# Performance work log

Measured on AMD Instinct MI355X. Metric: run time of the kernel, lower is better.

Reference implementation:

```python
import jax, jax.numpy as jnp
import numpy as np

KERNEL_SIZE = 4  # kernel_size=4, dim=1, degree-1 open B-splines (SplineConv defaults)


def spline_conv(x, edge_index, edge_attr, W, root, bias):
    """SplineConv with dim=1, kernel_size=4, degree=1, open splines, aggr='mean'.

    x: [N, F_in]; edge_index: [2, E] (row 0 = source, row 1 = target);
    edge_attr: [E, 1] pseudo-coords in [0,1]; W: [K, F_in, F_out];
    root: [F_in, F_out]; bias: [F_out].
    """
    N = x.shape[0]
    src, dst = edge_index[0], edge_index[1]
    u = edge_attr[:, 0]                          # [E]
    v = u * (KERNEL_SIZE - 1)                    # open spline: scale by K-1
    vf = jnp.floor(v)
    frac = v - vf                                # [E], degree-1 basis fraction
    k0 = jnp.clip(vf.astype(jnp.int32), 0, KERNEL_SIZE - 1)
    k1 = jnp.minimum(k0 + 1, KERNEL_SIZE - 1)
    # Project node features through all K kernel weights once: [N, K, F_out]
    xw = jnp.einsum('nf,kfo->nko', x, W)
    # Per-edge message: basis-weighted mix of the two active kernel projections
    m = (1.0 - frac)[:, None] * xw[src, k0] + frac[:, None] * xw[src, k1]  # [E, F_out]
    # Mean aggregation at target nodes
    agg = jax.ops.segment_sum(m, dst, num_segments=N)               # [N, F_out]
    deg = jax.ops.segment_sum(jnp.ones_like(u), dst, num_segments=N)
    agg = agg / jnp.maximum(deg, 1.0)[:, None]
    return agg + x @ root + bias


def setup_inputs() -> dict:
    key = jax.random.key(0)
    ks = jax.random.split(key, 9)
    N, E, F_IN, HID, C = 50000, 1600000, 48, 32, 10
    x = jax.random.normal(ks[0], (N, F_IN), dtype=jnp.float32)
    edge_index = jax.random.randint(ks[1], (2, E), 0, N, dtype=jnp.int64)
    edge_attr = jax.random.uniform(ks[2], (E, 1), dtype=jnp.float32)
    s = 0.1
    W1 = jax.random.normal(ks[3], (KERNEL_SIZE, F_IN, HID), dtype=jnp.float32) * s
    root1 = jax.random.normal(ks[4], (F_IN, HID), dtype=jnp.float32) * s
    bias1 = jax.random.normal(ks[5], (HID,), dtype=jnp.float32) * s
    W2 = jax.random.normal(ks[6], (KERNEL_SIZE, HID, C), dtype=jnp.float32) * s
    root2 = jax.random.normal(ks[7], (HID, C), dtype=jnp.float32) * s
    bias2 = jax.random.normal(ks[8], (C,), dtype=jnp.float32) * s
    return {"x": x, "edge_index": edge_index, "edge_attr": edge_attr,
            "W1": W1, "root1": root1, "bias1": bias1,
            "W2": W2, "root2": root2, "bias2": bias2}


def reference(x, edge_index, edge_attr, W1, root1, bias1, W2, root2, bias2):
    # dropout is identity in eval mode (training=self.training)
    h = spline_conv(x, edge_index, edge_attr, W1, root1, bias1)
    h = jax.nn.elu(h)
    h = spline_conv(h, edge_index, edge_attr, W2, root2, bias2)
    return jax.nn.log_softmax(h, axis=1)
```

## Files before the change

### kernel.cpp

```cpp
#include <hip/hip_runtime.h>
#include <math.h>


#define F_IN   48
#define HID    32
#define NCLS   10
#define KS     4
#define BKT_SH 8
#define TILE   4096

__device__ inline unsigned short f2bf(float f) {
    unsigned x = __float_as_uint(f);
    unsigned r = x + 0x7FFFu + ((x >> 16) & 1u);
    return (unsigned short)(r >> 16);
}
__device__ inline float bf2f(unsigned short u) {
    return __uint_as_float(((unsigned)u) << 16);
}


__global__ void bucket_hist_kernel(const int* __restrict__ ei, int* __restrict__ bcnt,
                                   int E, int NB) {
    __shared__ int lcnt[256];
    int t = threadIdx.x;
    lcnt[t] = 0;
    __syncthreads();
    int e0 = blockIdx.x * TILE;
    int n = min(TILE, E - e0);
    for (int r = 0; r < TILE / 256; ++r) {
        int i = r * 256 + t;
        if (i < n) atomicAdd(&lcnt[ei[E + e0 + i] >> BKT_SH], 1);
    }
    __syncthreads();
    if (t < NB && lcnt[t] > 0) atomicAdd(&bcnt[t], lcnt[t]);
}

__global__ void mini_scan_kernel(const int* __restrict__ bcnt, int* __restrict__ bbase,
                                 int* __restrict__ gcur, int NB) {
    __shared__ int a[256], c[256];
    int t = threadIdx.x;
    int v = (t < NB) ? bcnt[t] : 0;
    a[t] = v; c[t] = v;
    __syncthreads();
    for (int o = 1; o < 256; o <<= 1) {
        int w = (t >= o) ? a[t - o] : 0;
        __syncthreads();
        a[t] += w;
        __syncthreads();
    }
    int ex = a[t] - c[t];
    if (t < NB) { bbase[t] = ex; gcur[t] = ex; }
    if (t == 0) bbase[NB] = a[255];
}

__global__ void bucket_scatter_kernel(const int* __restrict__ ei, const float* __restrict__ ea,
                                      int* __restrict__ gcur, uint2* __restrict__ tpd,
                                      int E, int NB) {
    __shared__ unsigned spl[TILE];
    __shared__ unsigned short sdst[TILE];
    __shared__ unsigned short inv[TILE];
    __shared__ int lcnt[256], loff[256], lrank[256], gb[256];
    int t = threadIdx.x;
    lcnt[t] = 0; lrank[t] = 0;
    __syncthreads();
    int e0 = blockIdx.x * TILE;
    int n = min(TILE, E - e0);
    for (int r = 0; r < TILE / 256; ++r) {
        int i = r * 256 + t;
        if (i < n) {
            int e = e0 + i;
            int src = ei[e];
            int dst = ei[E + e];
            float u = ea[e];
            float v = u * (float)(KS - 1);
            float vf = floorf(v);
            int k0 = min(max((int)vf, 0), KS - 1);
            unsigned qf = (unsigned)((v - vf) * 16383.f + 0.5f);
            spl[i] = (unsigned)src | ((unsigned)k0 << 16) | (qf << 18);
            sdst[i] = (unsigned short)dst;
            atomicAdd(&lcnt[dst >> BKT_SH], 1);
        }
    }
    __syncthreads();
    loff[t] = lcnt[t];
    __syncthreads();
    for (int o = 1; o < 256; o <<= 1) {
        int w = (t >= o) ? loff[t - o] : 0;
        __syncthreads();
        loff[t] += w;
        __syncthreads();
    }
    int ex = loff[t] - lcnt[t];
    __syncthreads();
    loff[t] = ex;
    if (t < NB) gb[t] = atomicAdd(&gcur[t], lcnt[t]);
    __syncthreads();
    for (int r = 0; r < TILE / 256; ++r) {
        int i = r * 256 + t;
        if (i < n) {
            int b = sdst[i] >> BKT_SH;
            int p = loff[b] + atomicAdd(&lrank[b], 1);
            inv[p] = (unsigned short)i;
        }
    }
    __syncthreads();
    for (int r = 0; r < TILE / 256; ++r) {
        int j = r * 256 + t;
        if (j < n) {
            int i = inv[j];
            int d = sdst[i];
            int b = d >> BKT_SH;
            int pos = gb[b] + (j - loff[b]);
            tpd[pos] = make_uint2(spl[i], (unsigned)d);
        }
    }
}

__global__ void node_sort_kernel(const uint2* __restrict__ tpd, const int* __restrict__ bbase,
                                 unsigned* __restrict__ spk, int* __restrict__ offs,
                                 int N, int NB) {
    __shared__ int hc[256], hs[256], hr[256];
    int b = blockIdx.x;
    int t = threadIdx.x;
    int nb0 = b << BKT_SH;
    int nb = min(256, N - nb0);
    int base = bbase[b];
    int m = bbase[b + 1] - base;
    hc[t] = 0; hr[t] = 0;
    __syncthreads();
    for (int i = t; i < m; i += 256) atomicAdd(&hc[tpd[base + i].y - nb0], 1);
    __syncthreads();
    hs[t] = hc[t];
    __syncthreads();
    for (int o = 1; o < 256; o <<= 1) {
        int w = (t >= o) ? hs[t - o] : 0;
        __syncthreads();
        hs[t] += w;
        __syncthreads();
    }
    if (t < nb) offs[nb0 + t] = base + (hs[t] - hc[t]);
    if (b == NB - 1 && t == 0) offs[N] = base + m;
    for (int i = t; i < m; i += 256) {
        uint2 rec = tpd[base + i];
        int d = rec.y - nb0;
        int p = (hs[d] - hc[d]) + atomicAdd(&hr[d], 1);
        spk[base + p] = rec.x;
    }
}


__global__ __launch_bounds__(320) void xw1_kernel(
        const float* __restrict__ X, const float* __restrict__ W,
        const float* __restrict__ R, unsigned short* __restrict__ outk,
        float* __restrict__ outr, int n) {
    __shared__ float lw[48 * 160];
    int t = threadIdx.x;
    for (int i = t; i < 48 * 160; i += 320) {
        int f = i / 160;
        int col = i - f * 160;
        lw[i] = (col < 128) ? W[(size_t)(col >> 5) * (48 * 32) + f * 32 + (col & 31)]
                            : R[f * 32 + (col - 128)];
    }
    __syncthreads();
    int g = t % 40;
    int lp = t / 40;
    int n0 = (blockIdx.x * 8 + lp) * 2;
    if (n0 + 1 >= n) return;
    const float4* X0 = (const float4*)(X + (size_t)n0 * F_IN);
    const float4* X1 = (const float4*)(X + (size_t)(n0 + 1) * F_IN);
    float4 x0[12], x1[12];
#pragma unroll
    for (int i = 0; i < 12; ++i) { x0[i] = X0[i]; x1[i] = X1[i]; }
    const float4* lw4 = (const float4*)lw;
    float4 a0 = {0,0,0,0}, a1 = {0,0,0,0};
#pragma unroll
    for (int fb = 0; fb < 12; ++fb) {
        float4 v0 = x0[fb], v1 = x1[fb];
#pragma unroll
        for (int j = 0; j < 4; ++j) {
            float s0 = (j == 0) ? v0.x : (j == 1) ? v0.y : (j == 2) ? v0.z : v0.w;
            float s1 = (j == 0) ? v1.x : (j == 1) ? v1.y : (j == 2) ? v1.z : v1.w;
            float4 w = lw4[(fb * 4 + j) * 40 + g];
            a0.x = fmaf(s0, w.x, a0.x); a0.y = fmaf(s0, w.y, a0.y);
            a0.z = fmaf(s0, w.z, a0.z); a0.w = fmaf(s0, w.w, a0.w);
            a1.x = fmaf(s1, w.x, a1.x); a1.y = fmaf(s1, w.y, a1.y);
            a1.z = fmaf(s1, w.z, a1.z); a1.w = fmaf(s1, w.w, a1.w);
        }
    }
    if (g < 32) {
        uint2 u0, u1;
        u0.x = f2bf(a0.x) | ((unsigned)f2bf(a0.y) << 16);
        u0.y = f2bf(a0.z) | ((unsigned)f2bf(a0.w) << 16);
        u1.x = f2bf(a1.x) | ((unsigned)f2bf(a1.y) << 16);
        u1.y = f2bf(a1.z) | ((unsigned)f2bf(a1.w) << 16);
        *(uint2*)(outk + (size_t)n0 * (KS * HID) + g * 4) = u0;
        *(uint2*)(outk + (size_t)(n0 + 1) * (KS * HID) + g * 4) = u1;
    } else {
        int o = 4 * g - 128;
        *(float4*)(outr + (size_t)n0 * HID + o) = a0;
        *(float4*)(outr + (size_t)(n0 + 1) * HID + o) = a1;
    }
}

__global__ void xw2_kernel(const float* __restrict__ H, const float* __restrict__ W,
                           const float* __restrict__ R, unsigned short* __restrict__ outk,
                           float* __restrict__ outr, int n) {
    __shared__ float lw2[32 * 50];
    int t = threadIdx.x;
    for (int i = t; i < 32 * 50; i += 256) {
        int f = i / 50;
        int col = i - f * 50;
        lw2[i] = (col < 40) ? W[(size_t)(col / 10) * (32 * 10) + f * 10 + (col % 10)]
                            : R[f * 10 + (col - 40)];
    }
    __syncthreads();
    int total = (n / 2) * 25;
    int id = blockIdx.x * blockDim.x + t;
    if (id >= total) return;
    int p = id % 25;
    int pr = id / 25;
    int n0 = 2 * pr;
    const float4* H0 = (const float4*)(H + (size_t)n0 * HID);
    const float4* H1 = (const float4*)(H + (size_t)(n0 + 1) * HID);
    float4 h0[8], h1[8];
#pragma unroll
    for (int i = 0; i < 8; ++i) { h0[i] = H0[i]; h1[i] = H1[i]; }
    const float2* lwp = (const float2*)lw2;
    float ax0 = 0.f, ay0 = 0.f, ax1 = 0.f, ay1 = 0.f;
#pragma unroll
    for (int fb = 0; fb < 8; ++fb) {
        float4 v0 = h0[fb], v1 = h1[fb];
#pragma unroll
        for (int j = 0; j < 4; ++j) {
            float s0 = (j == 0) ? v0.x : (j == 1) ? v0.y : (j == 2) ? v0.z : v0.w;
            float s1 = (j == 0) ? v1.x : (j == 1) ? v1.y : (j == 2) ? v1.z : v1.w;
            float2 w = lwp[(fb * 4 + j) * 25 + p];
            ax0 = fmaf(s0, w.x, ax0); ay0 = fmaf(s0, w.y, ay0);
            ax1 = fmaf(s1, w.x, ax1); ay1 = fmaf(s1, w.y, ay1);
        }
    }
    int col = 2 * p;
    if (col < KS * NCLS) {
        *(unsigned*)(outk + (size_t)n0 * (KS * NCLS) + col) =
            f2bf(ax0) | ((unsigned)f2bf(ay0) << 16);
        *(unsigned*)(outk + (size_t)(n0 + 1) * (KS * NCLS) + col) =
            f2bf(ax1) | ((unsigned)f2bf(ay1) << 16);
    } else {
        int o = col - KS * NCLS;
        *(float2*)(outr + (size_t)n0 * NCLS + o) = make_float2(ax0, ay0);
        *(float2*)(outr + (size_t)(n0 + 1) * NCLS + o) = make_float2(ax1, ay1);
    }
}


#define DECODE32(p, row, dk, fr)                                          \
    {   int src_ = (p) & 0xFFFF;                                          \
        int k0_ = ((p) >> 16) & 3;                                        \
        int k1_ = min(k0_ + 1, KS - 1);                                   \
        fr = (float)((p) >> 18) * (1.f / 16383.f);                        \
        row = xwk + (size_t)src_ * (KS * HID) + k0_ * HID + cg * 4;       \
        dk = (k1_ - k0_) * HID; }

__device__ inline void fma4(uint2 v0, uint2 v1, float fr, float4& a) {
    float w0 = 1.f - fr;
    a.x = fmaf(w0, __uint_as_float(v0.x << 16), a.x);
    a.x = fmaf(fr, __uint_as_float(v1.x << 16), a.x);
    a.y = fmaf(w0, __uint_as_float(v0.x & 0xFFFF0000u), a.y);
    a.y = fmaf(fr, __uint_as_float(v1.x & 0xFFFF0000u), a.y);
    a.z = fmaf(w0, __uint_as_float(v0.y << 16), a.z);
    a.z = fmaf(fr, __uint_as_float(v1.y << 16), a.z);
    a.w = fmaf(w0, __uint_as_float(v0.y & 0xFFFF0000u), a.w);
    a.w = fmaf(fr, __uint_as_float(v1.y & 0xFFFF0000u), a.w);
}

__global__ void agg1_kernel(const unsigned short* __restrict__ xwk,
                            const float* __restrict__ xroot,
                            const int* __restrict__ offs, const unsigned* __restrict__ spk,
                            const float* __restrict__ bias, float* __restrict__ h, int n) {
    int lane = threadIdx.x & 63;
    int cg = lane & 7;
    int slot = lane >> 3;
    int node = blockIdx.x * 4 + (threadIdx.x >> 6);
    if (node >= n) return;
    int beg = offs[node];
    int end = offs[node + 1];
    float4 a0 = {0, 0, 0, 0}, a1 = {0, 0, 0, 0};
    int e = beg + slot;
    while (e + 24 < end) {
        unsigned p0 = spk[e], p1 = spk[e + 8], p2 = spk[e + 16], p3 = spk[e + 24];
        const unsigned short *r0, *r1, *r2, *r3;
        int d0, d1, d2, d3;
        float f0, f1, f2, f3;
        DECODE32(p0, r0, d0, f0);
        DECODE32(p1, r1, d1, f1);
        DECODE32(p2, r2, d2, f2);
        DECODE32(p3, r3, d3, f3);
        uint2 v00 = *(const uint2*)r0, v01 = *(const uint2*)(r0 + d0);
        uint2 v10 = *(const uint2*)r1, v11 = *(const uint2*)(r1 + d1);
        uint2 v20 = *(const uint2*)r2, v21 = *(const uint2*)(r2 + d2);
        uint2 v30 = *(const uint2*)r3, v31 = *(const uint2*)(r3 + d3);
        fma4(v00, v01, f0, a0);
        fma4(v10, v11, f1, a1);
        fma4(v20, v21, f2, a0);
        fma4(v30, v31, f3, a1);
        e += 32;
    }
    while (e < end) {
        unsigned p = spk[e];
        const unsigned short* r;
        int d;
        float f;
        DECODE32(p, r, d, f);
        uint2 v0 = *(const uint2*)r, v1 = *(const uint2*)(r + d);
        fma4(v0, v1, f, a0);
        e += 8;
    }
    float4 s;
    s.x = a0.x + a1.x; s.y = a0.y + a1.y; s.z = a0.z + a1.z; s.w = a0.w + a1.w;
#pragma unroll
    for (int m = 8; m < 64; m <<= 1) {
        s.x += __shfl_xor(s.x, m, 64);
        s.y += __shfl_xor(s.y, m, 64);
        s.z += __shfl_xor(s.z, m, 64);
        s.w += __shfl_xor(s.w, m, 64);
    }
    if (slot == 0) {
        int deg = end - beg;
        float inv = 1.f / (float)(deg > 0 ? deg : 1);
        float4 r = *(const float4*)(xroot + (size_t)node * HID + cg * 4);
        float4 b = *(const float4*)(bias + cg * 4);
        float4 o;
        o.x = fmaf(s.x, inv, r.x + b.x);
        o.y = fmaf(s.y, inv, r.y + b.y);
        o.z = fmaf(s.z, inv, r.z + b.z);
        o.w = fmaf(s.w, inv, r.w + b.w);
        o.x = (o.x > 0.f) ? o.x : expm1f(o.x);
        o.y = (o.y > 0.f) ? o.y : expm1f(o.y);
        o.z = (o.z > 0.f) ? o.z : expm1f(o.z);
        o.w = (o.w > 0.f) ? o.w : expm1f(o.w);
        *(float4*)(h + (size_t)node * HID + cg * 4) = o;
    }
}

#define DECODE10(p, row, dk, fr)                                          \
    {   int src_ = (p) & 0xFFFF;                                          \
        int k0_ = ((p) >> 16) & 3;                                        \
        int k1_ = min(k0_ + 1, KS - 1);                                   \
        fr = (float)((p) >> 18) * (1.f / 16383.f);                        \
        row = xwk + (size_t)src_ * (KS * NCLS) + k0_ * NCLS + cc;         \
        dk = (k1_ - k0_) * NCLS; }

__global__ void agg2_kernel(const unsigned short* __restrict__ xwk,
                            const float* __restrict__ xroot,
                            const int* __restrict__ offs, const unsigned* __restrict__ spk,
                            const float* __restrict__ bias, float* __restrict__ out, int n) {
    int lane = threadIdx.x & 63;
    int c = lane & 15;
    int slot = lane >> 4;
    int node = blockIdx.x * 4 + (threadIdx.x >> 6);
    if (node >= n) return;
    int cc = min(c, NCLS - 1);
    int beg = offs[node];
    int end = offs[node + 1];
    float s0 = 0.f, s1 = 0.f;
    int e = beg + slot;
    while (e + 12 < end) {
        unsigned p0 = spk[e], p1 = spk[e + 4], p2 = spk[e + 8], p3 = spk[e + 12];
        const unsigned short *r0, *r1, *r2, *r3;
        int d0, d1, d2, d3;
        float f0, f1, f2, f3;
        DECODE10(p0, r0, d0, f0);
        DECODE10(p1, r1, d1, f1);
        DECODE10(p2, r2, d2, f2);
        DECODE10(p3, r3, d3, f3);
        unsigned short a00 = r0[0], a01 = r0[d0];
        unsigned short a10 = r1[0], a11 = r1[d1];
        unsigned short a20 = r2[0], a21 = r2[d2];
        unsigned short a30 = r3[0], a31 = r3[d3];
        float x00 = bf2f(a00), x01 = bf2f(a01);
        float x10 = bf2f(a10), x11 = bf2f(a11);
        float x20 = bf2f(a20), x21 = bf2f(a21);
        float x30 = bf2f(a30), x31 = bf2f(a31);
        s0 += fmaf(f0, x01 - x00, x00);
        s1 += fmaf(f1, x11 - x10, x10);
        s0 += fmaf(f2, x21 - x20, x20);
        s1 += fmaf(f3, x31 - x30, x30);
        e += 16;
    }
    while (e < end) {
        unsigned p = spk[e];
        const unsigned short* r;
        int d;
        float f;
        DECODE10(p, r, d, f);
        float x0 = bf2f(r[0]), x1 = bf2f(r[d]);
        s0 += fmaf(f, x1 - x0, x0);
        e += 4;
    }
    float sum = s0 + s1;
    sum += __shfl_xor(sum, 16, 64);
    sum += __shfl_xor(sum, 32, 64);
    int deg = end - beg;
    float m = sum / (float)(deg > 0 ? deg : 1);
    float logit = m + xroot[(size_t)node * NCLS + cc] + bias[cc];
    bool active = (c < NCLS);
    float mx = active ? logit : -INFINITY;
#pragma unroll
    for (int msk = 1; msk < 16; msk <<= 1) mx = fmaxf(mx, __shfl_xor(mx, msk, 16));
    float ex = active ? expf(logit - mx) : 0.f;
    float s = ex;
#pragma unroll
    for (int msk = 1; msk < 16; msk <<= 1) s += __shfl_xor(s, msk, 16);
    if (active && slot == 0) out[(size_t)node * NCLS + c] = (logit - mx) - logf(s);
}

extern "C" void kernel_launch(void* const* d_in, const int* in_sizes, int n_in,
                              void* d_out, int out_size, void* d_ws, size_t ws_size,
                              hipStream_t stream) {
    const float* x       = (const float*)d_in[0];
    const int*   ei      = (const int*)d_in[1];
    const float* ea      = (const float*)d_in[2];
    const float* W1      = (const float*)d_in[3];
    const float* root1   = (const float*)d_in[4];
    const float* bias1   = (const float*)d_in[5];
    const float* W2      = (const float*)d_in[6];
    const float* root2   = (const float*)d_in[7];
    const float* bias2   = (const float*)d_in[8];
    float* out = (float*)d_out;

    const int N = in_sizes[0] / F_IN;
    const int E = in_sizes[2];
    const int NB = (N + 255) >> BKT_SH;

    char* base = (char*)d_ws;
    size_t off = 0;
    auto alloc = [&](size_t bytes) {
        char* p = base + off;
        off = (off + bytes + 255) & ~(size_t)255;
        return (void*)p;
    };
    unsigned short* xwk1 = (unsigned short*)alloc((size_t)N * KS * HID * 2);
    float* xr1           = (float*)alloc((size_t)N * HID * 4);
    float* h             = (float*)alloc((size_t)N * HID * 4);
    int* offs            = (int*)alloc(((size_t)N + 1) * 4);
    int* bcnt            = (int*)alloc((size_t)NB * 4);
    int* bbase           = (int*)alloc(((size_t)NB + 1) * 4);
    int* gcur            = (int*)alloc((size_t)NB * 4);
    unsigned* spk        = (unsigned*)alloc((size_t)E * 4);
    uint2* tpd           = (uint2*)xwk1;
    unsigned short* xwk2 = xwk1;
    float* xr2           = xr1;
    if (ws_size < off) return;

    int ebk = (E + TILE - 1) / TILE;

    hipMemsetAsync(bcnt, 0, (size_t)NB * 4, stream);
    bucket_hist_kernel<<<ebk, 256, 0, stream>>>(ei, bcnt, E, NB);
    mini_scan_kernel<<<1, 256, 0, stream>>>(bcnt, bbase, gcur, NB);
    bucket_scatter_kernel<<<ebk, 256, 0, stream>>>(ei, ea, gcur, tpd, E, NB);
    node_sort_kernel<<<NB, 256, 0, stream>>>(tpd, bbase, spk, offs, N, NB);
    xw1_kernel<<<(N + 15) / 16, 320, 0, stream>>>(x, W1, root1, xwk1, xr1, N);
    agg1_kernel<<<(N + 3) / 4, 256, 0, stream>>>(xwk1, xr1, offs, spk, bias1, h, N);
    {
        int total = (N / 2) * 25;
        xw2_kernel<<<(total + 255) / 256, 256, 0, stream>>>(h, W2, root2, xwk2, xr2, N);
    }
    agg2_kernel<<<(N + 3) / 4, 256, 0, stream>>>(xwk2, xr2, offs, spk, bias2, out, N);
}
```

Before: 250.1 us.

## Store layer-1 kernel projections as scaled FP8 with per-lane grouped layout

Layer 1 now quantizes the per-node kernel projections to FP8 (e4m3) after scaling by 16, instead of bf16. The row layout is regrouped so each lane's four kernel slices sit in one 16-byte chunk. The agg1 gather unpacks them with the hardware FP8-to-f32 conversion and folds the inverse scale into the mean normalization. This halves the bytes gathered per edge and keeps both basis reads in the same small chunk, reducing memory traffic in the edge aggregation. The cost is a coarser 3-bit mantissa, which may push the output past accuracy tolerance.

```diff
diff --git a/kernel.cpp b/kernel.cpp
--- a/kernel.cpp
+++ b/kernel.cpp
@@ -8,6 +8,9 @@
 #define KS     4
 #define BKT_SH 8
 #define TILE   4096
+#define FP8SC  16.f
+
+typedef float floatx2 __attribute__((ext_vector_type(2)));
 
 __device__ inline unsigned short f2bf(float f) {
     unsigned x = __float_as_uint(f);
@@ -151,7 +154,7 @@
 
 __global__ __launch_bounds__(320) void xw1_kernel(
         const float* __restrict__ X, const float* __restrict__ W,
-        const float* __restrict__ R, unsigned short* __restrict__ outk,
+        const float* __restrict__ R, unsigned char* __restrict__ outk,
         float* __restrict__ outr, int n) {
     __shared__ float lw[48 * 160];
     int t = threadIdx.x;
@@ -188,13 +191,13 @@
         }
     }
     if (g < 32) {
-        uint2 u0, u1;
-        u0.x = f2bf(a0.x) | ((unsigned)f2bf(a0.y) << 16);
-        u0.y = f2bf(a0.z) | ((unsigned)f2bf(a0.w) << 16);
-        u1.x = f2bf(a1.x) | ((unsigned)f2bf(a1.y) << 16);
-        u1.y = f2bf(a1.z) | ((unsigned)f2bf(a1.w) << 16);
-        *(uint2*)(outk + (size_t)n0 * (KS * HID) + g * 4) = u0;
-        *(uint2*)(outk + (size_t)(n0 + 1) * (KS * HID) + g * 4) = u1;
+        int off = (g & 7) * 16 + (g >> 3) * 4;
+        unsigned q0 = __builtin_amdgcn_cvt_pk_fp8_f32(a0.x * FP8SC, a0.y * FP8SC, 0, 0);
+        q0 = __builtin_amdgcn_cvt_pk_fp8_f32(a0.z * FP8SC, a0.w * FP8SC, q0, 1);
+        unsigned q1 = __builtin_amdgcn_cvt_pk_fp8_f32(a1.x * FP8SC, a1.y * FP8SC, 0, 0);
+        q1 = __builtin_amdgcn_cvt_pk_fp8_f32(a1.z * FP8SC, a1.w * FP8SC, q1, 1);
+        *(unsigned*)(outk + (size_t)n0 * 128 + off) = q0;
+        *(unsigned*)(outk + (size_t)(n0 + 1) * 128 + off) = q1;
     } else {
         int o = 4 * g - 128;
         *(float4*)(outr + (size_t)n0 * HID + o) = a0;
@@ -253,27 +256,27 @@
 }
 
 
-#define DECODE32(p, row, dk, fr)                                          \
+#define DECODE8(p, bp, o0, o1, fr)                                        \
     {   int src_ = (p) & 0xFFFF;                                          \
         int k0_ = ((p) >> 16) & 3;                                        \
         int k1_ = min(k0_ + 1, KS - 1);                                   \
         fr = (float)((p) >> 18) * (1.f / 16383.f);                        \
-        row = xwk + (size_t)src_ * (KS * HID) + k0_ * HID + cg * 4;       \
-        dk = (k1_ - k0_) * HID; }
-
-__device__ inline void fma4(uint2 v0, uint2 v1, float fr, float4& a) {
+        bp = xwk + (size_t)src_ * 128 + cg * 16;                          \
+        o0 = k0_ * 4; o1 = k1_ * 4; }
+
+__device__ inline void fma8(unsigned t0, unsigned t1, float fr, float4& a) {
     float w0 = 1.f - fr;
-    a.x = fmaf(w0, __uint_as_float(v0.x << 16), a.x);
-    a.x = fmaf(fr, __uint_as_float(v1.x << 16), a.x);
-    a.y = fmaf(w0, __uint_as_float(v0.x & 0xFFFF0000u), a.y);
-    a.y = fmaf(fr, __uint_as_float(v1.x & 0xFFFF0000u), a.y);
-    a.z = fmaf(w0, __uint_as_float(v0.y << 16), a.z);
-    a.z = fmaf(fr, __uint_as_float(v1.y << 16), a.z);
-    a.w = fmaf(w0, __uint_as_float(v0.y & 0xFFFF0000u), a.w);
-    a.w = fmaf(fr, __uint_as_float(v1.y & 0xFFFF0000u), a.w);
-}
-
-__global__ void agg1_kernel(const unsigned short* __restrict__ xwk,
+    floatx2 l0 = __builtin_amdgcn_cvt_pk_f32_fp8(t0, false);
+    floatx2 h0 = __builtin_amdgcn_cvt_pk_f32_fp8(t0, true);
+    floatx2 l1 = __builtin_amdgcn_cvt_pk_f32_fp8(t1, false);
+    floatx2 h1 = __builtin_amdgcn_cvt_pk_f32_fp8(t1, true);
+    a.x = fmaf(w0, l0.x, a.x); a.x = fmaf(fr, l1.x, a.x);
+    a.y = fmaf(w0, l0.y, a.y); a.y = fmaf(fr, l1.y, a.y);
+    a.z = fmaf(w0, h0.x, a.z); a.z = fmaf(fr, h1.x, a.z);
+    a.w = fmaf(w0, h0.y, a.w); a.w = fmaf(fr, h1.y, a.w);
+}
+
+__global__ void agg1_kernel(const unsigned char* __restrict__ xwk,
                             const float* __restrict__ xroot,
                             const int* __restrict__ offs, const unsigned* __restrict__ spk,
                             const float* __restrict__ bias, float* __restrict__ h, int n) {
@@ -288,31 +291,31 @@
     int e = beg + slot;
     while (e + 24 < end) {
         unsigned p0 = spk[e], p1 = spk[e + 8], p2 = spk[e + 16], p3 = spk[e + 24];
-        const unsigned short *r0, *r1, *r2, *r3;
-        int d0, d1, d2, d3;
+        const unsigned char *b0, *b1, *b2, *b3;
+        int o00, o01, o10, o11, o20, o21, o30, o31;
         float f0, f1, f2, f3;
-        DECODE32(p0, r0, d0, f0);
-        DECODE32(p1, r1, d1, f1);
-        DECODE32(p2, r2, d2, f2);
-        DECODE32(p3, r3, d3, f3);
-        uint2 v00 = *(const uint2*)r0, v01 = *(const uint2*)(r0 + d0);
-        uint2 v10 = *(const uint2*)r1, v11 = *(const uint2*)(r1 + d1);
-        uint2 v20 = *(const uint2*)r2, v21 = *(const uint2*)(r2 + d2);
-        uint2 v30 = *(const uint2*)r3, v31 = *(const uint2*)(r3 + d3);
-        fma4(v00, v01, f0, a0);
-        fma4(v10, v11, f1, a1);
-        fma4(v20, v21, f2, a0);
-        fma4(v30, v31, f3, a1);
+        DECODE8(p0, b0, o00, o01, f0);
+        DECODE8(p1, b1, o10, o11, f1);
+        DECODE8(p2, b2, o20, o21, f2);
+        DECODE8(p3, b3, o30, o31, f3);
+        unsigned t00 = *(const unsigned*)(b0 + o00), t01 = *(const unsigned*)(b0 + o01);
+        unsigned t10 = *(const unsigned*)(b1 + o10), t11 = *(const unsigned*)(b1 + o11);
+        unsigned t20 = *(const unsigned*)(b2 + o20), t21 = *(const unsigned*)(b2 + o21);
+        unsigned t30 = *(const unsigned*)(b3 + o30), t31 = *(const unsigned*)(b3 + o31);
+        fma8(t00, t01, f0, a0);
+        fma8(t10, t11, f1, a1);
+        fma8(t20, t21, f2, a0);
+        fma8(t30, t31, f3, a1);
         e += 32;
     }
     while (e < end) {
         unsigned p = spk[e];
-        const unsigned short* r;
-        int d;
+        const unsigned char* bp;
+        int o0, o1;
         float f;
-        DECODE32(p, r, d, f);
-        uint2 v0 = *(const uint2*)r, v1 = *(const uint2*)(r + d);
-        fma4(v0, v1, f, a0);
+        DECODE8(p, bp, o0, o1, f);
+        unsigned t0 = *(const unsigned*)(bp + o0), t1 = *(const unsigned*)(bp + o1);
+        fma8(t0, t1, f, a0);
         e += 8;
     }
     float4 s;
@@ -326,7 +329,7 @@
     }
     if (slot == 0) {
         int deg = end - beg;
-        float inv = 1.f / (float)(deg > 0 ? deg : 1);
+        float inv = (1.f / FP8SC) / (float)(deg > 0 ? deg : 1);
         float4 r = *(const float4*)(xroot + (size_t)node * HID + cg * 4);
         float4 b = *(const float4*)(bias + cg * 4);
         float4 o;
@@ -439,16 +442,16 @@
         off = (off + bytes + 255) & ~(size_t)255;
         return (void*)p;
     };
-    unsigned short* xwk1 = (unsigned short*)alloc((size_t)N * KS * HID * 2);
-    float* xr1           = (float*)alloc((size_t)N * HID * 4);
-    float* h             = (float*)alloc((size_t)N * HID * 4);
-    int* offs            = (int*)alloc(((size_t)N + 1) * 4);
-    int* bcnt            = (int*)alloc((size_t)NB * 4);
-    int* bbase           = (int*)alloc(((size_t)NB + 1) * 4);
-    int* gcur            = (int*)alloc((size_t)NB * 4);
-    unsigned* spk        = (unsigned*)alloc((size_t)E * 4);
-    uint2* tpd           = (uint2*)xwk1;
-    unsigned short* xwk2 = xwk1;
+    unsigned char* xwk1 = (unsigned char*)alloc((size_t)N * 128);
+    float* xr1          = (float*)alloc((size_t)N * HID * 4);
+    float* h            = (float*)alloc((size_t)N * HID * 4);
+    int* offs           = (int*)alloc(((size_t)N + 1) * 4);
+    int* bcnt           = (int*)alloc((size_t)NB * 4);
+    int* bbase          = (int*)alloc(((size_t)NB + 1) * 4);
+    int* gcur           = (int*)alloc((size_t)NB * 4);
+    unsigned* spk       = (unsigned*)alloc((size_t)E * 4);
+    uint2* tpd          = (uint2*)xwk1;
+    unsigned short* xwk2 = (unsigned short*)xwk1;
     float* xr2           = xr1;
     if (ws_size < off) return;
 
```

After: 251.8 us. About the same (+0.7%).

## Replace two-level bucket sort with atomic per-node CSR build

Applied to the files above, without the earlier changes.

Replaces the bucketed two-pass counting sort (bucket histogram, bucket scatter through a temporary buffer, per-bucket node sort) with a direct CSR build. The new path does a per-node degree histogram with global atomics, a three-kernel prefix scan, and an edge scatter that claims slots with a global atomicAdd on a per-node cursor. This removes the intermediate tpd buffer pass and the shared-memory shuffling. In exchange it relies on heavy global atomic traffic with random scatter writes, and edge order within each node becomes nondeterministic, so floating-point summation order can change between runs.

```diff
diff --git a/kernel.cpp b/kernel.cpp
--- a/kernel.cpp
+++ b/kernel.cpp
@@ -6,8 +6,6 @@
 #define HID    32
 #define NCLS   10
 #define KS     4
-#define BKT_SH 8
-#define TILE   4096
 
 __device__ inline unsigned short f2bf(float f) {
     unsigned x = __float_as_uint(f);
@@ -19,28 +17,28 @@
 }
 
 
-__global__ void bucket_hist_kernel(const int* __restrict__ ei, int* __restrict__ bcnt,
-                                   int E, int NB) {
-    __shared__ int lcnt[256];
+__global__ void deg_hist_kernel(const int* __restrict__ ei, int* __restrict__ deg, int E) {
+    int i = blockIdx.x * blockDim.x + threadIdx.x;
+    if (i < E) atomicAdd(&deg[ei[E + i]], 1);
+}
+
+__global__ void scan_a_kernel(const int* __restrict__ deg, int* __restrict__ bsum, int N) {
+    int i = blockIdx.x * 256 + threadIdx.x;
     int t = threadIdx.x;
-    lcnt[t] = 0;
+    int v = (i < N) ? deg[i] : 0;
+#pragma unroll
+    for (int m = 1; m < 64; m <<= 1) v += __shfl_xor(v, m, 64);
+    __shared__ int red[4];
+    if ((t & 63) == 0) red[t >> 6] = v;
     __syncthreads();
-    int e0 = blockIdx.x * TILE;
-    int n = min(TILE, E - e0);
-    for (int r = 0; r < TILE / 256; ++r) {
-        int i = r * 256 + t;
-        if (i < n) atomicAdd(&lcnt[ei[E + e0 + i] >> BKT_SH], 1);
-    }
-    __syncthreads();
-    if (t < NB && lcnt[t] > 0) atomicAdd(&bcnt[t], lcnt[t]);
-}
-
-__global__ void mini_scan_kernel(const int* __restrict__ bcnt, int* __restrict__ bbase,
-                                 int* __restrict__ gcur, int NB) {
-    __shared__ int a[256], c[256];
+    if (t == 0) bsum[blockIdx.x] = red[0] + red[1] + red[2] + red[3];
+}
+
+__global__ void scan_b_kernel(const int* __restrict__ bsum, int* __restrict__ bbase, int nb) {
+    __shared__ int a[256];
     int t = threadIdx.x;
-    int v = (t < NB) ? bcnt[t] : 0;
-    a[t] = v; c[t] = v;
+    int v = (t < nb) ? bsum[t] : 0;
+    a[t] = v;
     __syncthreads();
     for (int o = 1; o < 256; o <<= 1) {
         int w = (t >= o) ? a[t - o] : 0;
@@ -48,104 +46,42 @@
         a[t] += w;
         __syncthreads();
     }
-    int ex = a[t] - c[t];
-    if (t < NB) { bbase[t] = ex; gcur[t] = ex; }
-    if (t == 0) bbase[NB] = a[255];
-}
-
-__global__ void bucket_scatter_kernel(const int* __restrict__ ei, const float* __restrict__ ea,
-                                      int* __restrict__ gcur, uint2* __restrict__ tpd,
-                                      int E, int NB) {
-    __shared__ unsigned spl[TILE];
-    __shared__ unsigned short sdst[TILE];
-    __shared__ unsigned short inv[TILE];
-    __shared__ int lcnt[256], loff[256], lrank[256], gb[256];
+    if (t < nb) bbase[t] = a[t] - v;
+}
+
+__global__ void scan_c_kernel(const int* __restrict__ deg, const int* __restrict__ bbase,
+                              int* __restrict__ offs, int* __restrict__ cur, int N, int E) {
+    __shared__ int a[256];
     int t = threadIdx.x;
-    lcnt[t] = 0; lrank[t] = 0;
-    __syncthreads();
-    int e0 = blockIdx.x * TILE;
-    int n = min(TILE, E - e0);
-    for (int r = 0; r < TILE / 256; ++r) {
-        int i = r * 256 + t;
-        if (i < n) {
-            int e = e0 + i;
-            int src = ei[e];
-            int dst = ei[E + e];
-            float u = ea[e];
-            float v = u * (float)(KS - 1);
-            float vf = floorf(v);
-            int k0 = min(max((int)vf, 0), KS - 1);
-            unsigned qf = (unsigned)((v - vf) * 16383.f + 0.5f);
-            spl[i] = (unsigned)src | ((unsigned)k0 << 16) | (qf << 18);
-            sdst[i] = (unsigned short)dst;
-            atomicAdd(&lcnt[dst >> BKT_SH], 1);
-        }
-    }
-    __syncthreads();
-    loff[t] = lcnt[t];
+    int i = blockIdx.x * 256 + t;
+    int v = (i < N) ? deg[i] : 0;
+    a[t] = v;
     __syncthreads();
     for (int o = 1; o < 256; o <<= 1) {
-        int w = (t >= o) ? loff[t - o] : 0;
+        int w = (t >= o) ? a[t - o] : 0;
         __syncthreads();
-        loff[t] += w;
+        a[t] += w;
         __syncthreads();
     }
-    int ex = loff[t] - lcnt[t];
-    __syncthreads();
-    loff[t] = ex;
-    if (t < NB) gb[t] = atomicAdd(&gcur[t], lcnt[t]);
-    __syncthreads();
-    for (int r = 0; r < TILE / 256; ++r) {
-        int i = r * 256 + t;
-        if (i < n) {
-            int b = sdst[i] >> BKT_SH;
-            int p = loff[b] + atomicAdd(&lrank[b], 1);
-            inv[p] = (unsigned short)i;
-        }
-    }
-    __syncthreads();
-    for (int r = 0; r < TILE / 256; ++r) {
-        int j = r * 256 + t;
-        if (j < n) {
-            int i = inv[j];
-            int d = sdst[i];
-            int b = d >> BKT_SH;
-            int pos = gb[b] + (j - loff[b]);
-            tpd[pos] = make_uint2(spl[i], (unsigned)d);
-        }
-    }
-}
-
-__global__ void node_sort_kernel(const uint2* __restrict__ tpd, const int* __restrict__ bbase,
-                                 unsigned* __restrict__ spk, int* __restrict__ offs,
-                                 int N, int NB) {
-    __shared__ int hc[256], hs[256], hr[256];
-    int b = blockIdx.x;
-    int t = threadIdx.x;
-    int nb0 = b << BKT_SH;
-    int nb = min(256, N - nb0);
-    int base = bbase[b];
-    int m = bbase[b + 1] - base;
-    hc[t] = 0; hr[t] = 0;
-    __syncthreads();
-    for (int i = t; i < m; i += 256) atomicAdd(&hc[tpd[base + i].y - nb0], 1);
-    __syncthreads();
-    hs[t] = hc[t];
-    __syncthreads();
-    for (int o = 1; o < 256; o <<= 1) {
-        int w = (t >= o) ? hs[t - o] : 0;
-        __syncthreads();
-        hs[t] += w;
-        __syncthreads();
-    }
-    if (t < nb) offs[nb0 + t] = base + (hs[t] - hc[t]);
-    if (b == NB - 1 && t == 0) offs[N] = base + m;
-    for (int i = t; i < m; i += 256) {
-        uint2 rec = tpd[base + i];
-        int d = rec.y - nb0;
-        int p = (hs[d] - hc[d]) + atomicAdd(&hr[d], 1);
-        spk[base + p] = rec.x;
-    }
+    int ex = bbase[blockIdx.x] + a[t] - v;
+    if (i < N) { offs[i] = ex; cur[i] = ex; }
+    if (i == N - 1) offs[N] = E;
+}
+
+__global__ void edge_scatter_kernel(const int* __restrict__ ei, const float* __restrict__ ea,
+                                    int* __restrict__ cur, unsigned* __restrict__ spk, int E) {
+    int i = blockIdx.x * blockDim.x + threadIdx.x;
+    if (i >= E) return;
+    int src = ei[i];
+    int dst = ei[E + i];
+    float u = ea[i];
+    float v = u * (float)(KS - 1);
+    float vf = floorf(v);
+    int k0 = min(max((int)vf, 0), KS - 1);
+    unsigned qf = (unsigned)((v - vf) * 16383.f + 0.5f);
+    unsigned spl = (unsigned)src | ((unsigned)k0 << 16) | (qf << 18);
+    int pos = atomicAdd(&cur[dst], 1);
+    spk[pos] = spl;
 }
 
 
@@ -430,7 +366,7 @@
 
     const int N = in_sizes[0] / F_IN;
     const int E = in_sizes[2];
-    const int NB = (N + 255) >> BKT_SH;
+    const int NBLK = (N + 255) >> 8;
 
     char* base = (char*)d_ws;
     size_t off = 0;
@@ -443,22 +379,21 @@
     float* xr1           = (float*)alloc((size_t)N * HID * 4);
     float* h             = (float*)alloc((size_t)N * HID * 4);
     int* offs            = (int*)alloc(((size_t)N + 1) * 4);
-    int* bcnt            = (int*)alloc((size_t)NB * 4);
-    int* bbase           = (int*)alloc(((size_t)NB + 1) * 4);
-    int* gcur            = (int*)alloc((size_t)NB * 4);
+    int* deg             = (int*)alloc((size_t)N * 4);
+    int* cur             = (int*)alloc((size_t)N * 4);
+    int* bsum            = (int*)alloc((size_t)NBLK * 4);
+    int* bbase           = (int*)alloc((size_t)NBLK * 4);
     unsigned* spk        = (unsigned*)alloc((size_t)E * 4);
-    uint2* tpd           = (uint2*)xwk1;
     unsigned short* xwk2 = xwk1;
     float* xr2           = xr1;
     if (ws_size < off) return;
 
-    int ebk = (E + TILE - 1) / TILE;
-
-    hipMemsetAsync(bcnt, 0, (size_t)NB * 4, stream);
-    bucket_hist_kernel<<<ebk, 256, 0, stream>>>(ei, bcnt, E, NB);
-    mini_scan_kernel<<<1, 256, 0, stream>>>(bcnt, bbase, gcur, NB);
-    bucket_scatter_kernel<<<ebk, 256, 0, stream>>>(ei, ea, gcur, tpd, E, NB);
-    node_sort_kernel<<<NB, 256, 0, stream>>>(tpd, bbase, spk, offs, N, NB);
+    hipMemsetAsync(deg, 0, (size_t)N * 4, stream);
+    deg_hist_kernel<<<(E + 255) / 256, 256, 0, stream>>>(ei, deg, E);
+    scan_a_kernel<<<NBLK, 256, 0, stream>>>(deg, bsum, N);
+    scan_b_kernel<<<1, 256, 0, stream>>>(bsum, bbase, NBLK);
+    scan_c_kernel<<<NBLK, 256, 0, stream>>>(deg, bbase, offs, cur, N, E);
+    edge_scatter_kernel<<<(E + 255) / 256, 256, 0, stream>>>(ei, ea, cur, spk, E);
     xw1_kernel<<<(N + 15) / 16, 320, 0, stream>>>(x, W1, root1, xwk1, xr1, N);
     agg1_kernel<<<(N + 3) / 4, 256, 0, stream>>>(xwk1, xr1, offs, spk, bias1, h, N);
     {
```

After: 390.0 us. +56.0%, slower.

## Fuse layer-2 projection into agg1 and vectorize agg2 gathers

Applied to the files above, without the earlier changes.

The layer-2 projection (xw2) now runs inside agg1: each wavefront shuffles its ELU output across lanes and multiplies by W2/root2 staged in shared memory. This removes the h round-trip through global memory and one kernel launch. agg2 is remapped to 8 edge slots × 5 lanes, each lane loading a packed pair of bf16 values (uint32) rather than single 16-bit values. In exchange, every agg1 block reloads W2 into shared memory, and a __syncthreads is added before the main loop.

```diff
diff --git a/kernel.cpp b/kernel.cpp
--- a/kernel.cpp
+++ b/kernel.cpp
@@ -202,56 +202,6 @@
     }
 }
 
-__global__ void xw2_kernel(const float* __restrict__ H, const float* __restrict__ W,
-                           const float* __restrict__ R, unsigned short* __restrict__ outk,
-                           float* __restrict__ outr, int n) {
-    __shared__ float lw2[32 * 50];
-    int t = threadIdx.x;
-    for (int i = t; i < 32 * 50; i += 256) {
-        int f = i / 50;
-        int col = i - f * 50;
-        lw2[i] = (col < 40) ? W[(size_t)(col / 10) * (32 * 10) + f * 10 + (col % 10)]
-                            : R[f * 10 + (col - 40)];
-    }
-    __syncthreads();
-    int total = (n / 2) * 25;
-    int id = blockIdx.x * blockDim.x + t;
-    if (id >= total) return;
-    int p = id % 25;
-    int pr = id / 25;
-    int n0 = 2 * pr;
-    const float4* H0 = (const float4*)(H + (size_t)n0 * HID);
-    const float4* H1 = (const float4*)(H + (size_t)(n0 + 1) * HID);
-    float4 h0[8], h1[8];
-#pragma unroll
-    for (int i = 0; i < 8; ++i) { h0[i] = H0[i]; h1[i] = H1[i]; }
-    const float2* lwp = (const float2*)lw2;
-    float ax0 = 0.f, ay0 = 0.f, ax1 = 0.f, ay1 = 0.f;
-#pragma unroll
-    for (int fb = 0; fb < 8; ++fb) {
-        float4 v0 = h0[fb], v1 = h1[fb];
-#pragma unroll
-        for (int j = 0; j < 4; ++j) {
-            float s0 = (j == 0) ? v0.x : (j == 1) ? v0.y : (j == 2) ? v0.z : v0.w;
-            float s1 = (j == 0) ? v1.x : (j == 1) ? v1.y : (j == 2) ? v1.z : v1.w;
-            float2 w = lwp[(fb * 4 + j) * 25 + p];
-            ax0 = fmaf(s0, w.x, ax0); ay0 = fmaf(s0, w.y, ay0);
-            ax1 = fmaf(s1, w.x, ax1); ay1 = fmaf(s1, w.y, ay1);
-        }
-    }
-    int col = 2 * p;
-    if (col < KS * NCLS) {
-        *(unsigned*)(outk + (size_t)n0 * (KS * NCLS) + col) =
-            f2bf(ax0) | ((unsigned)f2bf(ay0) << 16);
-        *(unsigned*)(outk + (size_t)(n0 + 1) * (KS * NCLS) + col) =
-            f2bf(ax1) | ((unsigned)f2bf(ay1) << 16);
-    } else {
-        int o = col - KS * NCLS;
-        *(float2*)(outr + (size_t)n0 * NCLS + o) = make_float2(ax0, ay0);
-        *(float2*)(outr + (size_t)(n0 + 1) * NCLS + o) = make_float2(ax1, ay1);
-    }
-}
-
 
 #define DECODE32(p, row, dk, fr)                                          \
     {   int src_ = (p) & 0xFFFF;                                          \
@@ -276,12 +226,26 @@
 __global__ void agg1_kernel(const unsigned short* __restrict__ xwk,
                             const float* __restrict__ xroot,
                             const int* __restrict__ offs, const unsigned* __restrict__ spk,
-                            const float* __restrict__ bias, float* __restrict__ h, int n) {
-    int lane = threadIdx.x & 63;
+                            const float* __restrict__ bias,
+                            const float* __restrict__ W2, const float* __restrict__ R2,
+                            unsigned short* __restrict__ outk2, float* __restrict__ outr2,
+                            int n) {
+    __shared__ float lw2f[32 * 50];
+    int t = threadIdx.x;
+    for (int i = t; i < 32 * 50; i += 256) {
+        int f = i / 50;
+        int col = i - f * 50;
+        lw2f[i] = (col < 40) ? W2[(size_t)(col / 10) * (32 * 10) + f * 10 + (col % 10)]
+                             : R2[f * 10 + (col - 40)];
+    }
+    __syncthreads();
+
+    int lane = t & 63;
     int cg = lane & 7;
     int slot = lane >> 3;
-    int node = blockIdx.x * 4 + (threadIdx.x >> 6);
-    if (node >= n) return;
+    int node = blockIdx.x * 4 + (t >> 6);
+    bool nv = node < n;
+    if (!nv) node = n - 1;
     int beg = offs[node];
     int end = offs[node + 1];
     float4 a0 = {0, 0, 0, 0}, a1 = {0, 0, 0, 0};
@@ -324,94 +288,125 @@
         s.z += __shfl_xor(s.z, m, 64);
         s.w += __shfl_xor(s.w, m, 64);
     }
-    if (slot == 0) {
-        int deg = end - beg;
-        float inv = 1.f / (float)(deg > 0 ? deg : 1);
-        float4 r = *(const float4*)(xroot + (size_t)node * HID + cg * 4);
-        float4 b = *(const float4*)(bias + cg * 4);
-        float4 o;
-        o.x = fmaf(s.x, inv, r.x + b.x);
-        o.y = fmaf(s.y, inv, r.y + b.y);
-        o.z = fmaf(s.z, inv, r.z + b.z);
-        o.w = fmaf(s.w, inv, r.w + b.w);
-        o.x = (o.x > 0.f) ? o.x : expm1f(o.x);
-        o.y = (o.y > 0.f) ? o.y : expm1f(o.y);
-        o.z = (o.z > 0.f) ? o.z : expm1f(o.z);
-        o.w = (o.w > 0.f) ? o.w : expm1f(o.w);
-        *(float4*)(h + (size_t)node * HID + cg * 4) = o;
-    }
-}
-
-#define DECODE10(p, row, dk, fr)                                          \
-    {   int src_ = (p) & 0xFFFF;                                          \
-        int k0_ = ((p) >> 16) & 3;                                        \
-        int k1_ = min(k0_ + 1, KS - 1);                                   \
-        fr = (float)((p) >> 18) * (1.f / 16383.f);                        \
-        row = xwk + (size_t)src_ * (KS * NCLS) + k0_ * NCLS + cc;         \
-        dk = (k1_ - k0_) * NCLS; }
+    int deg = end - beg;
+    float invd = 1.f / (float)(deg > 0 ? deg : 1);
+    float4 r = *(const float4*)(xroot + (size_t)node * HID + cg * 4);
+    float4 b = *(const float4*)(bias + cg * 4);
+    float4 o;
+    o.x = fmaf(s.x, invd, r.x + b.x);
+    o.y = fmaf(s.y, invd, r.y + b.y);
+    o.z = fmaf(s.z, invd, r.z + b.z);
+    o.w = fmaf(s.w, invd, r.w + b.w);
+    o.x = (o.x > 0.f) ? o.x : expm1f(o.x);
+    o.y = (o.y > 0.f) ? o.y : expm1f(o.y);
+    o.z = (o.z > 0.f) ? o.z : expm1f(o.z);
+    o.w = (o.w > 0.f) ? o.w : expm1f(o.w);
+    int col = min(lane, 49);
+    int slbase = lane & 56;
+    float acc = 0.f;
+#pragma unroll
+    for (int fg = 0; fg < 8; ++fg) {
+        int sl = slbase | fg;
+        float h0 = __shfl(o.x, sl, 64);
+        float h1 = __shfl(o.y, sl, 64);
+        float h2 = __shfl(o.z, sl, 64);
+        float h3 = __shfl(o.w, sl, 64);
+        acc = fmaf(h0, lw2f[(4 * fg + 0) * 50 + col], acc);
+        acc = fmaf(h1, lw2f[(4 * fg + 1) * 50 + col], acc);
+        acc = fmaf(h2, lw2f[(4 * fg + 2) * 50 + col], acc);
+        acc = fmaf(h3, lw2f[(4 * fg + 3) * 50 + col], acc);
+    }
+    if (nv && lane < 50) {
+        if (col < 40) outk2[(size_t)node * 40 + col] = f2bf(acc);
+        else          outr2[(size_t)node * NCLS + (col - 40)] = acc;
+    }
+}
 
 __global__ void agg2_kernel(const unsigned short* __restrict__ xwk,
                             const float* __restrict__ xroot,
                             const int* __restrict__ offs, const unsigned* __restrict__ spk,
                             const float* __restrict__ bias, float* __restrict__ out, int n) {
     int lane = threadIdx.x & 63;
-    int c = lane & 15;
-    int slot = lane >> 4;
+    int u = lane & 7;
+    int slot = lane >> 3;
     int node = blockIdx.x * 4 + (threadIdx.x >> 6);
-    if (node >= n) return;
-    int cc = min(c, NCLS - 1);
+    bool nv = node < n;
+    if (!nv) node = n - 1;
+    int up = min(u, 4);
     int beg = offs[node];
     int end = offs[node + 1];
-    float s0 = 0.f, s1 = 0.f;
+    float a0l = 0.f, a0h = 0.f, a1l = 0.f, a1h = 0.f;
+
+#define DEC2(p, q0, q1, fr)                                               \
+    {   int src_ = (p) & 0xFFFF;                                          \
+        int k0_ = ((p) >> 16) & 3;                                        \
+        int k1_ = min(k0_ + 1, KS - 1);                                   \
+        fr = (float)((p) >> 18) * (1.f / 16383.f);                        \
+        const unsigned short* row_ = xwk + (size_t)src_ * 40;             \
+        q0 = (const unsigned*)(row_ + k0_ * 10) + up;                     \
+        q1 = (const unsigned*)(row_ + k1_ * 10) + up; }
+
+#define FMA2(t0, t1, fr, al, ah)                                          \
+    {   float w0_ = 1.f - fr;                                             \
+        al = fmaf(w0_, __uint_as_float((t0) << 16), al);                  \
+        al = fmaf(fr,  __uint_as_float((t1) << 16), al);                  \
+        ah = fmaf(w0_, __uint_as_float((t0) & 0xFFFF0000u), ah);          \
+        ah = fmaf(fr,  __uint_as_float((t1) & 0xFFFF0000u), ah); }
+
     int e = beg + slot;
-    while (e + 12 < end) {
-        unsigned p0 = spk[e], p1 = spk[e + 4], p2 = spk[e + 8], p3 = spk[e + 12];
-        const unsigned short *r0, *r1, *r2, *r3;
-        int d0, d1, d2, d3;
+    while (e + 24 < end) {
+        unsigned p0 = spk[e], p1 = spk[e + 8], p2 = spk[e + 16], p3 = spk[e + 24];
+        const unsigned *q00, *q01, *q10, *q11, *q20, *q21, *q30, *q31;
         float f0, f1, f2, f3;
-        DECODE10(p0, r0, d0, f0);
-        DECODE10(p1, r1, d1, f1);
-        DECODE10(p2, r2, d2, f2);
-        DECODE10(p3, r3, d3, f3);
-        unsigned short a00 = r0[0], a01 = r0[d0];
-        unsigned short a10 = r1[0], a11 = r1[d1];
-        unsigned short a20 = r2[0], a21 = r2[d2];
-        unsigned short a30 = r3[0], a31 = r3[d3];
-        float x00 = bf2f(a00), x01 = bf2f(a01);
-        float x10 = bf2f(a10), x11 = bf2f(a11);
-        float x20 = bf2f(a20), x21 = bf2f(a21);
-        float x30 = bf2f(a30), x31 = bf2f(a31);
-        s0 += fmaf(f0, x01 - x00, x00);
-        s1 += fmaf(f1, x11 - x10, x10);
-        s0 += fmaf(f2, x21 - x20, x20);
-        s1 += fmaf(f3, x31 - x30, x30);
-        e += 16;
+        DEC2(p0, q00, q01, f0);
+        DEC2(p1, q10, q11, f1);
+        DEC2(p2, q20, q21, f2);
+        DEC2(p3, q30, q31, f3);
+        unsigned t00 = *q00, t01 = *q01;
+        unsigned t10 = *q10, t11 = *q11;
+        unsigned t20 = *q20, t21 = *q21;
+        unsigned t30 = *q30, t31 = *q31;
+        FMA2(t00, t01, f0, a0l, a0h);
+        FMA2(t10, t11, f1, a1l, a1h);
+        FMA2(t20, t21, f2, a0l, a0h);
+        FMA2(t30, t31, f3, a1l, a1h);
+        e += 32;
     }
     while (e < end) {
         unsigned p = spk[e];
-        const unsigned short* r;
-        int d;
+        const unsigned *q0, *q1;
         float f;
-        DECODE10(p, r, d, f);
-        float x0 = bf2f(r[0]), x1 = bf2f(r[d]);
-        s0 += fmaf(f, x1 - x0, x0);
-        e += 4;
-    }
-    float sum = s0 + s1;
-    sum += __shfl_xor(sum, 16, 64);
-    sum += __shfl_xor(sum, 32, 64);
+        DEC2(p, q0, q1, f);
+        unsigned t0 = *q0, t1 = *q1;
+        FMA2(t0, t1, f, a0l, a0h);
+        e += 8;
+    }
+    float vl = a0l + a1l, vh = a0h + a1h;
+    if (u > 4) { vl = 0.f; vh = 0.f; }
+#pragma unroll
+    for (int m = 8; m < 64; m <<= 1) {
+        vl += __shfl_xor(vl, m, 64);
+        vh += __shfl_xor(vh, m, 64);
+    }
     int deg = end - beg;
-    float m = sum / (float)(deg > 0 ? deg : 1);
-    float logit = m + xroot[(size_t)node * NCLS + cc] + bias[cc];
-    bool active = (c < NCLS);
-    float mx = active ? logit : -INFINITY;
-#pragma unroll
-    for (int msk = 1; msk < 16; msk <<= 1) mx = fmaxf(mx, __shfl_xor(mx, msk, 16));
-    float ex = active ? expf(logit - mx) : 0.f;
-    float s = ex;
-#pragma unroll
-    for (int msk = 1; msk < 16; msk <<= 1) s += __shfl_xor(s, msk, 16);
-    if (active && slot == 0) out[(size_t)node * NCLS + c] = (logit - mx) - logf(s);
+    float invd = 1.f / (float)(deg > 0 ? deg : 1);
+    float l0 = -INFINITY, l1 = -INFINITY;
+    if (u < 5) {
+        float2 xr = *(const float2*)(xroot + (size_t)node * NCLS + 2 * u);
+        l0 = fmaf(vl, invd, xr.x + bias[2 * u]);
+        l1 = fmaf(vh, invd, xr.y + bias[2 * u + 1]);
+    }
+    float mx = fmaxf(l0, l1);
+#pragma unroll
+    for (int m = 1; m < 8; m <<= 1) mx = fmaxf(mx, __shfl_xor(mx, m, 64));
+    float sden = (u < 5) ? (expf(l0 - mx) + expf(l1 - mx)) : 0.f;
+#pragma unroll
+    for (int m = 1; m < 8; m <<= 1) sden += __shfl_xor(sden, m, 64);
+    if (nv && slot == 0 && u < 5) {
+        float ls = logf(sden);
+        *(float2*)(out + (size_t)node * NCLS + 2 * u) =
+            make_float2(l0 - mx - ls, l1 - mx - ls);
+    }
 }
 
 extern "C" void kernel_launch(void* const* d_in, const int* in_sizes, int n_in,
@@ -441,15 +436,14 @@
     };
     unsigned short* xwk1 = (unsigned short*)alloc((size_t)N * KS * HID * 2);
     float* xr1           = (float*)alloc((size_t)N * HID * 4);
-    float* h             = (float*)alloc((size_t)N * HID * 4);
+    unsigned short* xwk2 = (unsigned short*)alloc((size_t)N * 40 * 2);
+    float* xr2           = (float*)alloc((size_t)N * NCLS * 4);
     int* offs            = (int*)alloc(((size_t)N + 1) * 4);
     int* bcnt            = (int*)alloc((size_t)NB * 4);
     int* bbase           = (int*)alloc(((size_t)NB + 1) * 4);
     int* gcur            = (int*)alloc((size_t)NB * 4);
     unsigned* spk        = (unsigned*)alloc((size_t)E * 4);
     uint2* tpd           = (uint2*)xwk1;
-    unsigned short* xwk2 = xwk1;
-    float* xr2           = xr1;
     if (ws_size < off) return;
 
     int ebk = (E + TILE - 1) / TILE;
@@ -460,10 +454,7 @@
     bucket_scatter_kernel<<<ebk, 256, 0, stream>>>(ei, ea, gcur, tpd, E, NB);
     node_sort_kernel<<<NB, 256, 0, stream>>>(tpd, bbase, spk, offs, N, NB);
     xw1_kernel<<<(N + 15) / 16, 320, 0, stream>>>(x, W1, root1, xwk1, xr1, N);
-    agg1_kernel<<<(N + 3) / 4, 256, 0, stream>>>(xwk1, xr1, offs, spk, bias1, h, N);
-    {
-        int total = (N / 2) * 25;
-        xw2_kernel<<<(total + 255) / 256, 256, 0, stream>>>(h, W2, root2, xwk2, xr2, N);
-    }
+    agg1_kernel<<<(N + 3) / 4, 256, 0, stream>>>(xwk1, xr1, offs, spk, bias1,
+                                                 W2, root2, xwk2, xr2, N);
     agg2_kernel<<<(N + 3) / 4, 256, 0, stream>>>(xwk2, xr2, offs, spk, bias2, out, N);
 }
```

After: 258.4 us. 1.03x slower.
